# Performance work log

Measured on AMD Instinct MI355X. Metric: run time of the kernel, lower is better.

## Reference

```python
import math
import jax, jax.numpy as jnp
import numpy as np

B, S, F, I, K, L, C = 2, 2048, 512, 1024, 3, 2, 256
BETA = 0.99                 # momentumnet_beta
INIT_SCALE = L ** -0.5      # per-cell output scale
PI = math.pi


def setup_inputs() -> dict:
    key = jax.random.key(0)
    ks = jax.random.split(key, 8)
    inp = jax.random.randint(ks[0], (B, S), 0, C)
    tgt = jax.random.randint(ks[1], (B, S), 0, C)
    emb = jax.random.normal(ks[2], (C, 2 * F), jnp.float32) * 0.02
    w0s = jax.random.normal(ks[3], (L, 3, I, F, 1), jnp.float32) * (F ** -0.5)
    w1s = jax.random.normal(ks[4], (L, 3, I, I, K), jnp.float32) * ((I * K) ** -0.5)
    w2s = jax.random.normal(ks[5], (L, 3, F, I, 1), jnp.float32) * (I ** -0.5)
    out_w = jax.random.normal(ks[6], (C, 2 * F, 1), jnp.float32) * ((2 * F) ** -0.5)
    out_b = jax.random.normal(ks[7], (C,), jnp.float32) * 0.02
    return {"inp": inp, "tgt": tgt, "emb": emb, "w0s": w0s, "w1s": w1s,
            "w2s": w2s, "out_w": out_w, "out_b": out_b}


def causal_conv(x, w):
    # x: [B, Cin, S], w: [Cout, Cin, k]; left-pad k-1 (matches torch pad+(k-1,0)+conv1d)
    k = w.shape[-1]
    return jax.lax.conv_general_dilated(x, w, (1,), [(k - 1, 0)],
                                        dimension_numbers=("NCH", "OIH", "NCH"))


def feed_forward(x, w0, w1, w2):
    x = jax.nn.relu(causal_conv(x, w0))
    x = jax.nn.relu(causal_conv(x, w1))
    return causal_conv(x, w2)


def norm(x):
    # mean-subtract + RMS-style L2 norm over channel dim (dim 1)
    x = x - x.mean(1, keepdims=True)
    return x / (jnp.linalg.norm(x, axis=1, keepdims=True) * (x.shape[1] ** -0.5) + 1e-5)


def _feature_embd():
    f = jnp.arange(F, dtype=jnp.float32)[:, None] + 1.0
    additive = f % 2.0
    f = (f - additive) / 2.0
    f = f * (8.0 / F) - math.log(C / (2.0 * PI))
    return jnp.exp(f) + additive * PI  # [F, 1]


def _forward(inp, tgt, emb, w0s, w1s, w2s, out_w, out_b):
    fe = _feature_embd()
    divisor = (jnp.arange(S, dtype=jnp.float32) + 1.0)[None, None, :]  # [1,1,S]
    x = emb[inp].transpose(0, 2, 1)         # [B, 2F, S]
    a, b = x[:, :F], x[:, F:]               # reversible streams [B, F, S]
    for l in range(L):
        h = b + fe                          # training-path positional embedding
        d = feed_forward(h, w0s[l, 0], w1s[l, 0], w2s[l, 0])
        sc = feed_forward(h, w0s[l, 1], w1s[l, 1], w2s[l, 1])
        sh = feed_forward(h, w0s[l, 2], w1s[l, 2], w2s[l, 2])
        cum = jnp.cumsum(d, axis=1)         # cumsum over feature dim (dim 1, as in source)
        cell = norm(cum / divisor * sc + sh) * INIT_SCALE
        c = BETA * a + (1.0 - BETA) * cell  # momentum coupling forward
        a, b = c, b + c                     # Identity layer with additive coupling
    streams = jnp.concatenate([a, b], axis=1)        # [B, 2F, S]
    logits = causal_conv(streams, out_w) + out_b[None, :, None]  # [B, C, S]
    logp = jax.nn.log_softmax(logits, axis=1)
    nll = -jnp.take_along_axis(logp, tgt[:, None, :], axis=1)[:, 0, :]
    return nll.mean()                       # torch cross_entropy (mean reduction)


def reference(inp, tgt, emb, w0s, w1s, w2s, out_w, out_b):
    return _forward(inp, tgt, emb, w0s, w1s, w2s, out_w, out_b)
```

## Files before the change

### kernel.cpp

```cpp
#include <hip/hip_runtime.h>

#define S_ 2048
#define F_ 512
#define I_ 1024
#define C_ 256

typedef float f4 __attribute__((ext_vector_type(4)));
typedef __bf16 bf8 __attribute__((ext_vector_type(8)));
typedef __bf16 bf4 __attribute__((ext_vector_type(4)));
typedef int i4v __attribute__((ext_vector_type(4)));
typedef int i8v __attribute__((ext_vector_type(8)));
typedef unsigned char u8;

__device__ __forceinline__ void gload_lds16(const void* g, void* l) {
  __builtin_amdgcn_global_load_lds(
      (const __attribute__((address_space(1))) void*)g,
      (__attribute__((address_space(3))) void*)l, 16, 0, 0);
}

__device__ __forceinline__ float fe_val(int f) {
  const float PI_F = 3.14159265358979323846f;
  float additive = (f & 1) ? 0.0f : 1.0f;
  float fv = ((float)(f + 1) - additive) * 0.5f;
  fv = fv * (8.0f / (float)F_) - logf((float)C_ / (2.0f * PI_F));
  return expf(fv) + additive * PI_F;
}

template <int KW, bool RELU, int OUT, int NTILE, int KD, int LDB>
__global__ __launch_bounds__(256) void gemm_f8(
    const u8* __restrict__ Ab, const u8* __restrict__ Bb, void* __restrict__ Cb,
    const u8* __restrict__ zpage, int M, int PZ, long sAp, long sBp, long sBb,
    long sCz) {
  constexpr int NF = NTILE / 32;
  constexpr int NIT = KD / 128;
  constexpr int AK = KW * KD;
  constexpr int BG = NTILE / 32;
  __shared__ u8 Asm[16384];
  __shared__ u8 Bsm[NTILE * 128];
  const int tid = threadIdx.x;
  const int z = blockIdx.z;
  const int p = z % PZ;
  const int bb = z / PZ;
  const u8* A = Ab + (long)p * sAp;
  const u8* B = Bb + (long)bb * sBb + (long)p * sBp;
  const int m0 = blockIdx.y * 128;
  const int n0 = blockIdx.x * NTILE;
  const int lane = tid & 63;
  const int wave = tid >> 6;
  const int wr = wave >> 1;
  const int wc = wave & 1;
  const int l15 = lane & 15;
  const int quad = lane >> 4;
  const int srow = tid >> 2;
  const int sslot = tid & 3;
  const int sswz = sslot ^ ((srow >> 1) & 3);
  const int rsw = (l15 >> 1) & 3;
  const int s0 = ((quad & 1) << 1) ^ rsw;
  const int hbA = (quad >> 1) * 8192;
  const int hbB = (quad >> 1) * (NTILE * 64);
  f4 acc[4][NF] = {};

  const u8* pA[4];
#pragma unroll
  for (int g = 0; g < 4; ++g) {
    const int row = (g & 1) * 64 + srow;
    const int chunk = (g >> 1) * 4 + sswz;
    pA[g] = A + (long)(m0 + row) * AK + chunk * 16;
  }

  for (int t = 0; t < KW; ++t) {
    const u8* pB[BG];
#pragma unroll
    for (int g = 0; g < BG; ++g) {
      const int row = (BG == 4 ? (g & 1) * 64 : 0) + srow;
      const int chunk = (BG == 4 ? (g >> 1) : g) * 4 + sswz;
      const int rg = n0 + row + ((KW == 3) ? (t - 2) : 0);
      pB[g] = (KW == 3 && rg < 0) ? (zpage + chunk * 16)
                                  : (B + (long)rg * LDB + chunk * 16);
    }
    const long ka = (long)t * KD;
#pragma unroll 1
    for (int it = 0; it < NIT; ++it) {
      const int kb = it * 128;
#pragma unroll
      for (int g = 0; g < 4; ++g)
        gload_lds16(pA[g] + ka + kb, Asm + g * 4096 + wave * 1024);
#pragma unroll
      for (int g = 0; g < BG; ++g)
        gload_lds16(pB[g] + kb, Bsm + g * 4096 + wave * 1024);
      __syncthreads();
      i8v af[4], bfr[NF];
#pragma unroll
      for (int mt = 0; mt < 4; ++mt) {
        const u8* rp = Asm + hbA + (wr * 64 + mt * 16 + l15) * 64;
        const i4v lo = *(const i4v*)(rp + s0 * 16);
        const i4v hi = *(const i4v*)(rp + (s0 ^ 1) * 16);
        af[mt][0] = lo[0]; af[mt][1] = lo[1]; af[mt][2] = lo[2]; af[mt][3] = lo[3];
        af[mt][4] = hi[0]; af[mt][5] = hi[1]; af[mt][6] = hi[2]; af[mt][7] = hi[3];
      }
#pragma unroll
      for (int nt = 0; nt < NF; ++nt) {
        const u8* rp = Bsm + hbB + (wc * (NTILE / 2) + nt * 16 + l15) * 64;
        const i4v lo = *(const i4v*)(rp + s0 * 16);
        const i4v hi = *(const i4v*)(rp + (s0 ^ 1) * 16);
        bfr[nt][0] = lo[0]; bfr[nt][1] = lo[1]; bfr[nt][2] = lo[2]; bfr[nt][3] = lo[3];
        bfr[nt][4] = hi[0]; bfr[nt][5] = hi[1]; bfr[nt][6] = hi[2]; bfr[nt][7] = hi[3];
      }
#pragma unroll
      for (int mt = 0; mt < 4; ++mt)
#pragma unroll
        for (int nt = 0; nt < NF; ++nt)
          acc[mt][nt] = __builtin_amdgcn_mfma_scale_f32_16x16x128_f8f6f4(
              af[mt], bfr[nt], acc[mt][nt], 0, 0, 0, 0x7F7F7F7F, 0, 0x7F7F7F7F);
      __syncthreads();
    }
  }
#pragma unroll
  for (int mt = 0; mt < 4; ++mt) {
    const int m = m0 + wr * 64 + mt * 16 + quad * 4;
#pragma unroll
    for (int nt = 0; nt < NF; ++nt) {
      const int n = n0 + wc * (NTILE / 2) + nt * 16 + l15;
      f4 v = acc[mt][nt];
#pragma unroll
      for (int q = 0; q < 4; ++q) {
        v[q] *= 0.015625f;
        if (RELU) v[q] = fmaxf(v[q], 0.0f);
      }
      if (OUT == 2) {
        int r = __builtin_amdgcn_cvt_pk_fp8_f32(v[0], v[1], 0, false);
        r = __builtin_amdgcn_cvt_pk_fp8_f32(v[2], v[3], r, true);
        *(int*)((u8*)Cb + (long)z * sCz + (long)n * M + m) = r;
      } else {
        *(f4*)((float*)Cb + (long)z * sCz + (long)n * M + m) = v;
      }
    }
  }
}

__device__ __forceinline__ void cvt4(const float* __restrict__ s,
                                     __bf16* __restrict__ d, long T) {
  const long i = T * 4;
  const float4 v = *(const float4*)(s + i);
  bf4 o;
  o[0] = (__bf16)v.x;
  o[1] = (__bf16)v.y;
  o[2] = (__bf16)v.z;
  o[3] = (__bf16)v.w;
  *(bf4*)(d + i) = o;
}

__device__ __forceinline__ void cvt4f8(const float* __restrict__ s,
                                       u8* __restrict__ d, long T) {
  const long i = T * 4;
  const float4 v = *(const float4*)(s + i);
  int r = __builtin_amdgcn_cvt_pk_fp8_f32(v.x * 64.0f, v.y * 64.0f, 0, false);
  r = __builtin_amdgcn_cvt_pk_fp8_f32(v.z * 64.0f, v.w * 64.0f, r, true);
  *(int*)(d + i) = r;
}

__device__ __forceinline__ u8 to_fp8(float v) {
  return (u8)(__builtin_amdgcn_cvt_pk_fp8_f32(v, 0.0f, 0, false) & 0xFF);
}

__global__ void k_prep(const float* __restrict__ w0, const float* __restrict__ w2,
                       const float* __restrict__ ow, const float* __restrict__ w1,
                       u8* __restrict__ W0f8, u8* __restrict__ W2f8,
                       __bf16* __restrict__ OWc, u8* __restrict__ W1f8) {
  long T = (long)blockIdx.x * 256 + threadIdx.x;
  if (T < 786432L) {
    cvt4f8(w0, W0f8, T);
    return;
  }
  T -= 786432L;
  if (T < 786432L) {
    cvt4f8(w2, W2f8, T);
    return;
  }
  T -= 786432L;
  if (T < 65536L) {
    cvt4(ow, OWc, T);
    return;
  }
  T -= 65536L;
  const long j = T & (I_ - 1);
  const long r3 = T >> 10;
  const float* src = w1 + T * 3;
  u8* dst = W1f8 + r3 * 3072 + j;
  dst[0] = to_fp8(src[0] * 64.0f);
  dst[1024] = to_fp8(src[1] * 64.0f);
  dst[2048] = to_fp8(src[2] * 64.0f);
}

__global__ __launch_bounds__(64) void k_embed(const int* __restrict__ inp,
                                              const float* __restrict__ emb,
                                              float* __restrict__ a_st,
                                              float* __restrict__ b_st,
                                              u8* __restrict__ h) {
  const int col = blockIdx.x;
  const int lane = threadIdx.x;
  const int f0 = lane * 8;
  const float* e = emb + (long)inp[col] * (2 * F_);
  const float4 a0 = *(const float4*)(e + f0);
  const float4 a1 = *(const float4*)(e + f0 + 4);
  const float4 b0 = *(const float4*)(e + F_ + f0);
  const float4 b1 = *(const float4*)(e + F_ + f0 + 4);
  *(float4*)(a_st + (long)col * F_ + f0) = a0;
  *(float4*)(a_st + (long)col * F_ + f0 + 4) = a1;
  *(float4*)(b_st + (long)col * F_ + f0) = b0;
  *(float4*)(b_st + (long)col * F_ + f0 + 4) = b1;
  const float bb[8] = {b0.x, b0.y, b0.z, b0.w, b1.x, b1.y, b1.z, b1.w};
  float hv[8];
#pragma unroll
  for (int q = 0; q < 8; ++q) hv[q] = bb[q] + fe_val(f0 + q);
  int lo = __builtin_amdgcn_cvt_pk_fp8_f32(hv[0], hv[1], 0, false);
  lo = __builtin_amdgcn_cvt_pk_fp8_f32(hv[2], hv[3], lo, true);
  int hi = __builtin_amdgcn_cvt_pk_fp8_f32(hv[4], hv[5], 0, false);
  hi = __builtin_amdgcn_cvt_pk_fp8_f32(hv[6], hv[7], hi, true);
  *(int2*)(h + (long)col * F_ + f0) = {lo, hi};
}

__global__ __launch_bounds__(64) void k_cell(const float* __restrict__ Y3,
                                             float* __restrict__ a_st,
                                             float* __restrict__ b_st,
                                             void* __restrict__ outp,
                                             int last) {
  const int col = blockIdx.x;
  const int s = col & (S_ - 1);
  const int b = col >> 11;
  const int lane = threadIdx.x;
  const int f0 = lane * 8;
  const float* d = Y3 + ((long)(3 * b + 0) * S_ + s) * F_ + f0;
  const float* sc = Y3 + ((long)(3 * b + 1) * S_ + s) * F_ + f0;
  const float* sh = Y3 + ((long)(3 * b + 2) * S_ + s) * F_ + f0;
  float* ap = a_st + (long)col * F_ + f0;
  float* bp = b_st + (long)col * F_ + f0;
  const float inv_div = 1.0f / (float)(s + 1);

  const float4 d0 = *(const float4*)d;
  const float4 d1 = *(const float4*)(d + 4);
  const float4 sc0 = *(const float4*)sc;
  const float4 sc1 = *(const float4*)(sc + 4);
  const float4 sh0 = *(const float4*)sh;
  const float4 sh1 = *(const float4*)(sh + 4);

  float c[8];
  c[0] = d0.x;
  c[1] = c[0] + d0.y;
  c[2] = c[1] + d0.z;
  c[3] = c[2] + d0.w;
  c[4] = c[3] + d1.x;
  c[5] = c[4] + d1.y;
  c[6] = c[5] + d1.z;
  c[7] = c[6] + d1.w;
  const float tot = c[7];
  float scan = tot;
#pragma unroll
  for (int off = 1; off < 64; off <<= 1) {
    float nb = __shfl_up(scan, off);
    if (lane >= off) scan += nb;
  }
  const float base = scan - tot;

  float v[8];
  v[0] = (base + c[0]) * inv_div * sc0.x + sh0.x;
  v[1] = (base + c[1]) * inv_div * sc0.y + sh0.y;
  v[2] = (base + c[2]) * inv_div * sc0.z + sh0.z;
  v[3] = (base + c[3]) * inv_div * sc0.w + sh0.w;
  v[4] = (base + c[4]) * inv_div * sc1.x + sh1.x;
  v[5] = (base + c[5]) * inv_div * sc1.y + sh1.y;
  v[6] = (base + c[6]) * inv_div * sc1.z + sh1.z;
  v[7] = (base + c[7]) * inv_div * sc1.w + sh1.w;

  float sum = 0.f, ssq = 0.f;
#pragma unroll
  for (int q = 0; q < 8; ++q) {
    sum += v[q];
    ssq += v[q] * v[q];
  }
#pragma unroll
  for (int off = 1; off < 64; off <<= 1) {
    sum += __shfl_xor(sum, off);
    ssq += __shfl_xor(ssq, off);
  }
  const float mean = sum * (1.0f / (float)F_);
  const float nsq = fmaxf(ssq - (float)F_ * mean * mean, 0.0f);
  const float denom = sqrtf(nsq) * 0.04419417382415922f + 1e-5f;
  const float isc = 0.7071067811865476f / denom;

  const float4 av0 = *(const float4*)ap;
  const float4 av1 = *(const float4*)(ap + 4);
  const float4 bv0 = *(const float4*)bp;
  const float4 bv1 = *(const float4*)(bp + 4);
  float an[8], bn[8];
  const float ai[8] = {av0.x, av0.y, av0.z, av0.w, av1.x, av1.y, av1.z, av1.w};
  const float bi[8] = {bv0.x, bv0.y, bv0.z, bv0.w, bv1.x, bv1.y, bv1.z, bv1.w};
#pragma unroll
  for (int q = 0; q < 8; ++q) {
    const float cell = (v[q] - mean) * isc;
    an[q] = 0.99f * ai[q] + 0.01f * cell;
    bn[q] = bi[q] + an[q];
  }
  *(float4*)ap = {an[0], an[1], an[2], an[3]};
  *(float4*)(ap + 4) = {an[4], an[5], an[6], an[7]};
  *(float4*)bp = {bn[0], bn[1], bn[2], bn[3]};
  *(float4*)(bp + 4) = {bn[4], bn[5], bn[6], bn[7]};
  if (!last) {
    float hv[8];
#pragma unroll
    for (int q = 0; q < 8; ++q) hv[q] = bn[q] + fe_val(f0 + q);
    int lo = __builtin_amdgcn_cvt_pk_fp8_f32(hv[0], hv[1], 0, false);
    lo = __builtin_amdgcn_cvt_pk_fp8_f32(hv[2], hv[3], lo, true);
    int hi = __builtin_amdgcn_cvt_pk_fp8_f32(hv[4], hv[5], 0, false);
    hi = __builtin_amdgcn_cvt_pk_fp8_f32(hv[6], hv[7], hi, true);
    *(int2*)((u8*)outp + (long)col * F_ + f0) = {lo, hi};
  } else {
    bf8 oa, ob;
#pragma unroll
    for (int q = 0; q < 8; ++q) {
      oa[q] = (__bf16)an[q];
      ob[q] = (__bf16)bn[q];
    }
    *(bf8*)((__bf16*)outp + (long)col * (2 * F_) + f0) = oa;
    *(bf8*)((__bf16*)outp + (long)col * (2 * F_) + F_ + f0) = ob;
  }
}

__global__ __launch_bounds__(256) void k_logits_nll(
    const __bf16* __restrict__ A, const __bf16* __restrict__ Bb,
    const float* __restrict__ outb, const int* __restrict__ tgt,
    float* __restrict__ acc) {
  __shared__ __bf16 As[256 * 32];
  __shared__ __bf16 Bs[64 * 32];
  __shared__ float lsm[64 * 256];
  const int tid = threadIdx.x;
  const int b = blockIdx.y;
  const int n0 = blockIdx.x * 64;
  const __bf16* Bt = Bb + (long)b * (S_ * 2 * F_) + (long)n0 * (2 * F_);
  const int lane = tid & 63;
  const int wave = tid >> 6;
  const int l15 = lane & 15;
  const int quad = lane >> 4;
  const int cr = tid >> 2;
  const int csw = (((tid & 3) ^ ((cr >> 1) & 3)) << 3);
  const int roff = ((quad ^ ((l15 >> 1) & 3)) << 3);
  f4 av[4][4] = {};
  for (int k0 = 0; k0 < 2 * F_; k0 += 32) {
#pragma unroll
    for (int i = 0; i < 4; ++i)
      gload_lds16(A + (long)(i * 64 + cr) * (2 * F_) + (k0 + csw),
                  As + ((i * 256 + (wave << 6)) << 3));
    gload_lds16(Bt + (long)cr * (2 * F_) + (k0 + csw), Bs + ((wave << 6) << 3));
    __syncthreads();
    bf8 af[4], bfr[4];
#pragma unroll
    for (int mt = 0; mt < 4; ++mt)
      af[mt] = *(const bf8*)(As + (wave * 64 + mt * 16 + l15) * 32 + roff);
#pragma unroll
    for (int nt = 0; nt < 4; ++nt)
      bfr[nt] = *(const bf8*)(Bs + (nt * 16 + l15) * 32 + roff);
#pragma unroll
    for (int mt = 0; mt < 4; ++mt)
#pragma unroll
      for (int nt = 0; nt < 4; ++nt)
        av[mt][nt] = __builtin_amdgcn_mfma_f32_16x16x32_bf16(af[mt], bfr[nt],
                                                             av[mt][nt], 0, 0, 0);
    __syncthreads();
  }
#pragma unroll
  for (int mt = 0; mt < 4; ++mt) {
    const int m = wave * 64 + mt * 16 + quad * 4;
#pragma unroll
    for (int nt = 0; nt < 4; ++nt) {
      const int pp = nt * 16 + l15;
      *(f4*)(lsm + pp * C_ + m) = av[mt][nt];
    }
  }
  __syncthreads();
  const float4 bv = *(const float4*)(outb + lane * 4);
  float wsum = 0.f;
  for (int i = 0; i < 16; ++i) {
    const int pp = wave * 16 + i;
    const f4 lv = *(const f4*)(lsm + pp * C_ + lane * 4);
    const float x0 = lv[0] + bv.x, x1 = lv[1] + bv.y, x2 = lv[2] + bv.z,
                x3 = lv[3] + bv.w;
    float mx = fmaxf(fmaxf(x0, x1), fmaxf(x2, x3));
#pragma unroll
    for (int off = 1; off < 64; off <<= 1) mx = fmaxf(mx, __shfl_xor(mx, off));
    float ss = expf(x0 - mx) + expf(x1 - mx) + expf(x2 - mx) + expf(x3 - mx);
#pragma unroll
    for (int off = 1; off < 64; off <<= 1) ss += __shfl_xor(ss, off);
    if (lane == 0) {
      const int t = tgt[b * S_ + n0 + pp];
      wsum += mx + logf(ss) - (lsm[pp * C_ + t] + outb[t]);
    }
  }
  if (lane == 0) atomicAdd(acc, wsum);
}

__global__ void k_final(const float* __restrict__ acc, float* __restrict__ out) {
  out[0] = acc[0] * (1.0f / 4096.0f);
}

extern "C" void kernel_launch(void* const* d_in, const int* in_sizes, int n_in,
                              void* d_out, int out_size, void* d_ws,
                              size_t ws_size, hipStream_t stream) {
  const int* inp = (const int*)d_in[0];
  const int* tgt = (const int*)d_in[1];
  const float* emb = (const float*)d_in[2];
  const float* w0s = (const float*)d_in[3];
  const float* w1s = (const float*)d_in[4];
  const float* w2s = (const float*)d_in[5];
  const float* out_w = (const float*)d_in[6];
  const float* out_b = (const float*)d_in[7];

  char* ws = (char*)d_ws;
  float* acc = (float*)(ws + 0);
  u8* zp = (u8*)(ws + 256);
  float* a_st = (float*)(ws + 4096);
  float* b_st = (float*)(ws + 8392704L);
  u8* h = (u8*)(ws + 16781312L);
  u8* Y1f8 = (u8*)(ws + 20975616L);
  u8* Y2f8 = (u8*)(ws + 46141440L);
  float* Y3 = (float*)(ws + 71307264L);
  u8* W1f8 = (u8*)(ws + 96473088L);
  __bf16* streams = (__bf16*)(ws + 134221824L);
  u8* W0f8 = (u8*)(ws + 146804736L);
  u8* W2f8 = (u8*)(ws + 153096192L);
  __bf16* OWc = (__bf16*)(ws + 159387648L);

  hipMemsetAsync(ws, 0, 4096, stream);
  k_prep<<<30976, 256, 0, stream>>>(w0s, w2s, out_w, w1s, W0f8, W2f8, OWc, W1f8);
  k_embed<<<4096, 64, 0, stream>>>(inp, emb, a_st, b_st, h);

  for (int l = 0; l < 2; ++l) {
    gemm_f8<1, true, 2, 128, 512, 512><<<dim3(16, 24, 2), 256, 0, stream>>>(
        W0f8 + (long)l * 1572864L, h, Y1f8, zp, 3072, 1, 0L, 0L, 1048576L,
        6291456L);
    gemm_f8<3, true, 2, 128, 1024, 3072><<<dim3(16, 8, 6), 256, 0, stream>>>(
        W1f8 + (long)l * 9437184L, Y1f8, Y2f8, zp, 1024, 3, 3145728L, 1024L,
        6291456L, 2097152L);
    gemm_f8<1, false, 0, 64, 1024, 1024><<<dim3(32, 4, 6), 256, 0, stream>>>(
        W2f8 + (long)l * 1572864L, Y2f8, Y3, zp, 512, 3, 524288L, 2097152L,
        6291456L, 1048576L);
    k_cell<<<4096, 64, 0, stream>>>(Y3, a_st, b_st,
                                    (l == 0) ? (void*)h : (void*)streams,
                                    (l == 1) ? 1 : 0);
  }

  k_logits_nll<<<dim3(32, 2), 256, 0, stream>>>(OWc, streams, out_b, tgt, acc);
  k_final<<<1, 1, 0, stream>>>(acc, (float*)d_out);
}
```

Baseline: 368.0 us.

## Rework fp8 GEMM LDS layout, vectorize w1 conversion, halve logits tile

The fp8 GEMM shared-memory staging moves from split half-buffers of 64-byte rows to full 128-byte rows with an XOR swizzle over 8 chunks, which simplifies address math and is meant to cut LDS bank conflicts. The w1 weight conversion now reads float4s and writes packed 4-byte fp8 words in place of scattered single-byte stores, so the prep kernel launches fewer threads. The logits/NLL kernel uses 32-column tiles, doubling the grid to 128 blocks to fill more CUs, at the cost of loading the class weights more often.

Result: faster. 349.7 us (-5.0%).

```diff
diff --git a/kernel.cpp b/kernel.cpp
--- a/kernel.cpp
+++ b/kernel.cpp
@@ -34,8 +34,8 @@
   constexpr int NF = NTILE / 32;
   constexpr int NIT = KD / 128;
   constexpr int AK = KW * KD;
-  constexpr int BG = NTILE / 32;
-  __shared__ u8 Asm[16384];
+  constexpr int BP = NTILE / 32;
+  __shared__ u8 Asm[128 * 128];
   __shared__ u8 Bsm[NTILE * 128];
   const int tid = threadIdx.x;
   const int z = blockIdx.z;
@@ -51,58 +51,45 @@
   const int wc = wave & 1;
   const int l15 = lane & 15;
   const int quad = lane >> 4;
-  const int srow = tid >> 2;
-  const int sslot = tid & 3;
-  const int sswz = sslot ^ ((srow >> 1) & 3);
-  const int rsw = (l15 >> 1) & 3;
-  const int s0 = ((quad & 1) << 1) ^ rsw;
-  const int hbA = (quad >> 1) * 8192;
-  const int hbB = (quad >> 1) * (NTILE * 64);
+  const int cr = tid >> 3;
+  const int csw = (((tid & 7) ^ (cr & 7)) << 4);
+  const int off0 = (((2 * quad) ^ (l15 & 7)) << 4);
+  const int off1 = (((2 * quad + 1) ^ (l15 & 7)) << 4);
   f4 acc[4][NF] = {};
 
-  const u8* pA[4];
-#pragma unroll
-  for (int g = 0; g < 4; ++g) {
-    const int row = (g & 1) * 64 + srow;
-    const int chunk = (g >> 1) * 4 + sswz;
-    pA[g] = A + (long)(m0 + row) * AK + chunk * 16;
-  }
-
   for (int t = 0; t < KW; ++t) {
-    const u8* pB[BG];
-#pragma unroll
-    for (int g = 0; g < BG; ++g) {
-      const int row = (BG == 4 ? (g & 1) * 64 : 0) + srow;
-      const int chunk = (BG == 4 ? (g >> 1) : g) * 4 + sswz;
-      const int rg = n0 + row + ((KW == 3) ? (t - 2) : 0);
-      pB[g] = (KW == 3 && rg < 0) ? (zpage + chunk * 16)
-                                  : (B + (long)rg * LDB + chunk * 16);
-    }
-    const long ka = (long)t * KD;
+    const u8* pA = A + (long)t * KD;
+    const u8* pB[BP];
+#pragma unroll
+    for (int g = 0; g < BP; ++g) {
+      const int rg = n0 + g * 32 + cr + ((KW == 3) ? (t - 2) : 0);
+      pB[g] = (KW == 3 && rg < 0) ? (zpage + csw) : (B + (long)rg * LDB + csw);
+    }
 #pragma unroll 1
     for (int it = 0; it < NIT; ++it) {
       const int kb = it * 128;
 #pragma unroll
       for (int g = 0; g < 4; ++g)
-        gload_lds16(pA[g] + ka + kb, Asm + g * 4096 + wave * 1024);
-#pragma unroll
-      for (int g = 0; g < BG; ++g)
+        gload_lds16(pA + (long)(m0 + g * 32 + cr) * AK + kb + csw,
+                    Asm + g * 4096 + wave * 1024);
+#pragma unroll
+      for (int g = 0; g < BP; ++g)
         gload_lds16(pB[g] + kb, Bsm + g * 4096 + wave * 1024);
       __syncthreads();
       i8v af[4], bfr[NF];
 #pragma unroll
       for (int mt = 0; mt < 4; ++mt) {
-        const u8* rp = Asm + hbA + (wr * 64 + mt * 16 + l15) * 64;
-        const i4v lo = *(const i4v*)(rp + s0 * 16);
-        const i4v hi = *(const i4v*)(rp + (s0 ^ 1) * 16);
+        const u8* rp = Asm + (wr * 64 + mt * 16 + l15) * 128;
+        const i4v lo = *(const i4v*)(rp + off0);
+        const i4v hi = *(const i4v*)(rp + off1);
         af[mt][0] = lo[0]; af[mt][1] = lo[1]; af[mt][2] = lo[2]; af[mt][3] = lo[3];
         af[mt][4] = hi[0]; af[mt][5] = hi[1]; af[mt][6] = hi[2]; af[mt][7] = hi[3];
       }
 #pragma unroll
       for (int nt = 0; nt < NF; ++nt) {
-        const u8* rp = Bsm + hbB + (wc * (NTILE / 2) + nt * 16 + l15) * 64;
-        const i4v lo = *(const i4v*)(rp + s0 * 16);
-        const i4v hi = *(const i4v*)(rp + (s0 ^ 1) * 16);
+        const u8* rp = Bsm + (wc * (NTILE / 2) + nt * 16 + l15) * 128;
+        const i4v lo = *(const i4v*)(rp + off0);
+        const i4v hi = *(const i4v*)(rp + off1);
         bfr[nt][0] = lo[0]; bfr[nt][1] = lo[1]; bfr[nt][2] = lo[2]; bfr[nt][3] = lo[3];
         bfr[nt][4] = hi[0]; bfr[nt][5] = hi[1]; bfr[nt][6] = hi[2]; bfr[nt][7] = hi[3];
       }
@@ -159,8 +146,9 @@
   *(int*)(d + i) = r;
 }
 
-__device__ __forceinline__ u8 to_fp8(float v) {
-  return (u8)(__builtin_amdgcn_cvt_pk_fp8_f32(v, 0.0f, 0, false) & 0xFF);
+__device__ __forceinline__ int pk4f8(float a, float b, float c, float d) {
+  int r = __builtin_amdgcn_cvt_pk_fp8_f32(a, b, 0, false);
+  return __builtin_amdgcn_cvt_pk_fp8_f32(c, d, r, true);
 }
 
 __global__ void k_prep(const float* __restrict__ w0, const float* __restrict__ w2,
@@ -183,13 +171,16 @@
     return;
   }
   T -= 65536L;
-  const long j = T & (I_ - 1);
-  const long r3 = T >> 10;
-  const float* src = w1 + T * 3;
-  u8* dst = W1f8 + r3 * 3072 + j;
-  dst[0] = to_fp8(src[0] * 64.0f);
-  dst[1024] = to_fp8(src[1] * 64.0f);
-  dst[2048] = to_fp8(src[2] * 64.0f);
+  const long j4 = T & 255;
+  const long r3 = T >> 8;
+  const float* src = w1 + r3 * 3072 + j4 * 12;
+  const float4 v0 = *(const float4*)src;
+  const float4 v1 = *(const float4*)(src + 4);
+  const float4 v2 = *(const float4*)(src + 8);
+  u8* dst = W1f8 + r3 * 3072 + j4 * 4;
+  *(int*)(dst) = pk4f8(v0.x * 64.f, v0.w * 64.f, v1.z * 64.f, v2.y * 64.f);
+  *(int*)(dst + 1024) = pk4f8(v0.y * 64.f, v1.x * 64.f, v1.w * 64.f, v2.z * 64.f);
+  *(int*)(dst + 2048) = pk4f8(v0.z * 64.f, v1.y * 64.f, v2.x * 64.f, v2.w * 64.f);
 }
 
 __global__ __launch_bounds__(64) void k_embed(const int* __restrict__ inp,
@@ -213,10 +204,8 @@
   float hv[8];
 #pragma unroll
   for (int q = 0; q < 8; ++q) hv[q] = bb[q] + fe_val(f0 + q);
-  int lo = __builtin_amdgcn_cvt_pk_fp8_f32(hv[0], hv[1], 0, false);
-  lo = __builtin_amdgcn_cvt_pk_fp8_f32(hv[2], hv[3], lo, true);
-  int hi = __builtin_amdgcn_cvt_pk_fp8_f32(hv[4], hv[5], 0, false);
-  hi = __builtin_amdgcn_cvt_pk_fp8_f32(hv[6], hv[7], hi, true);
+  const int lo = pk4f8(hv[0], hv[1], hv[2], hv[3]);
+  const int hi = pk4f8(hv[4], hv[5], hv[6], hv[7]);
   *(int2*)(h + (long)col * F_ + f0) = {lo, hi};
 }
 
@@ -309,10 +298,8 @@
     float hv[8];
 #pragma unroll
     for (int q = 0; q < 8; ++q) hv[q] = bn[q] + fe_val(f0 + q);
-    int lo = __builtin_amdgcn_cvt_pk_fp8_f32(hv[0], hv[1], 0, false);
-    lo = __builtin_amdgcn_cvt_pk_fp8_f32(hv[2], hv[3], lo, true);
-    int hi = __builtin_amdgcn_cvt_pk_fp8_f32(hv[4], hv[5], 0, false);
-    hi = __builtin_amdgcn_cvt_pk_fp8_f32(hv[6], hv[7], hi, true);
+    const int lo = pk4f8(hv[0], hv[1], hv[2], hv[3]);
+    const int hi = pk4f8(hv[4], hv[5], hv[6], hv[7]);
     *(int2*)((u8*)outp + (long)col * F_ + f0) = {lo, hi};
   } else {
     bf8 oa, ob;
@@ -331,11 +318,11 @@
     const float* __restrict__ outb, const int* __restrict__ tgt,
     float* __restrict__ acc) {
   __shared__ __bf16 As[256 * 32];
-  __shared__ __bf16 Bs[64 * 32];
-  __shared__ float lsm[64 * 256];
+  __shared__ __bf16 Bs[32 * 32];
+  __shared__ float lsm[32 * 256];
   const int tid = threadIdx.x;
   const int b = blockIdx.y;
-  const int n0 = blockIdx.x * 64;
+  const int n0 = blockIdx.x * 32;
   const __bf16* Bt = Bb + (long)b * (S_ * 2 * F_) + (long)n0 * (2 * F_);
   const int lane = tid & 63;
   const int wave = tid >> 6;
@@ -344,25 +331,27 @@
   const int cr = tid >> 2;
   const int csw = (((tid & 3) ^ ((cr >> 1) & 3)) << 3);
   const int roff = ((quad ^ ((l15 >> 1) & 3)) << 3);
-  f4 av[4][4] = {};
+  f4 av[4][2] = {};
   for (int k0 = 0; k0 < 2 * F_; k0 += 32) {
 #pragma unroll
     for (int i = 0; i < 4; ++i)
       gload_lds16(A + (long)(i * 64 + cr) * (2 * F_) + (k0 + csw),
                   As + ((i * 256 + (wave << 6)) << 3));
-    gload_lds16(Bt + (long)cr * (2 * F_) + (k0 + csw), Bs + ((wave << 6) << 3));
+    if (wave < 2)
+      gload_lds16(Bt + (long)cr * (2 * F_) + (k0 + csw),
+                  Bs + ((wave << 6) << 3));
     __syncthreads();
-    bf8 af[4], bfr[4];
+    bf8 af[4], bfr[2];
 #pragma unroll
     for (int mt = 0; mt < 4; ++mt)
       af[mt] = *(const bf8*)(As + (wave * 64 + mt * 16 + l15) * 32 + roff);
 #pragma unroll
-    for (int nt = 0; nt < 4; ++nt)
+    for (int nt = 0; nt < 2; ++nt)
       bfr[nt] = *(const bf8*)(Bs + (nt * 16 + l15) * 32 + roff);
 #pragma unroll
     for (int mt = 0; mt < 4; ++mt)
 #pragma unroll
-      for (int nt = 0; nt < 4; ++nt)
+      for (int nt = 0; nt < 2; ++nt)
         av[mt][nt] = __builtin_amdgcn_mfma_f32_16x16x32_bf16(af[mt], bfr[nt],
                                                              av[mt][nt], 0, 0, 0);
     __syncthreads();
@@ -371,7 +360,7 @@
   for (int mt = 0; mt < 4; ++mt) {
     const int m = wave * 64 + mt * 16 + quad * 4;
 #pragma unroll
-    for (int nt = 0; nt < 4; ++nt) {
+    for (int nt = 0; nt < 2; ++nt) {
       const int pp = nt * 16 + l15;
       *(f4*)(lsm + pp * C_ + m) = av[mt][nt];
     }
@@ -379,8 +368,8 @@
   __syncthreads();
   const float4 bv = *(const float4*)(outb + lane * 4);
   float wsum = 0.f;
-  for (int i = 0; i < 16; ++i) {
-    const int pp = wave * 16 + i;
+  for (int i = 0; i < 8; ++i) {
+    const int pp = wave * 8 + i;
     const f4 lv = *(const f4*)(lsm + pp * C_ + lane * 4);
     const float x0 = lv[0] + bv.x, x1 = lv[1] + bv.y, x2 = lv[2] + bv.z,
                 x3 = lv[3] + bv.w;
@@ -430,7 +419,7 @@
   __bf16* OWc = (__bf16*)(ws + 159387648L);
 
   hipMemsetAsync(ws, 0, 4096, stream);
-  k_prep<<<30976, 256, 0, stream>>>(w0s, w2s, out_w, w1s, W0f8, W2f8, OWc, W1f8);
+  k_prep<<<12544, 256, 0, stream>>>(w0s, w2s, out_w, w1s, W0f8, W2f8, OWc, W1f8);
   k_embed<<<4096, 64, 0, stream>>>(inp, emb, a_st, b_st, h);
 
   for (int l = 0; l < 2; ++l) {
@@ -448,6 +437,6 @@
                                     (l == 1) ? 1 : 0);
   }
 
-  k_logits_nll<<<dim3(32, 2), 256, 0, stream>>>(OWc, streams, out_b, tgt, acc);
+  k_logits_nll<<<dim3(64, 2), 256, 0, stream>>>(OWc, streams, out_b, tgt, acc);
   k_final<<<1, 1, 0, stream>>>(acc, (float*)d_out);
 }
```
